# Kernel tuning notes

Hardware: AMD Instinct MI355X
Metric: run time of the kernel (lower is better)

The kernel has to match this reference:

```python
import jax, jax.numpy as jnp
import numpy as np

N_NODES = 100000
N_EDGES = 1600000
D_IN = 128
D_OUT = 5


def setup_inputs() -> dict:
    key = jax.random.key(0)
    k1, k2, k3, k4, k5 = jax.random.split(key, 5)
    x = jax.random.normal(k1, (N_NODES, D_IN), dtype=jnp.float32)
    edge_index = jax.random.randint(k2, (2, N_EDGES), 0, N_NODES, dtype=jnp.int64)
    scale = 1.0 / np.sqrt(D_IN)
    W_l = jax.random.normal(k3, (D_OUT, D_IN), dtype=jnp.float32) * scale
    b_l = jax.random.normal(k4, (D_OUT,), dtype=jnp.float32) * scale
    W_r = jax.random.normal(k5, (D_OUT, D_IN), dtype=jnp.float32) * scale
    return {"x": x, "edge_index": edge_index, "W_l": W_l, "b_l": b_l, "W_r": W_r}


def reference(x, edge_index, W_l, b_l, W_r):
    # PyG SAGEConv with aggr='mean', root_weight=True:
    # out_i = mean_{j: (j->i) in E} x_j @ W_l^T + b_l + x_i @ W_r^T
    n = x.shape[0]
    src = edge_index[0]
    dst = edge_index[1]
    msgs = x[src]  # [E, D_in] gather (irregular access)
    agg_sum = jax.ops.segment_sum(msgs, dst, num_segments=n)  # [N, D_in]
    deg = jax.ops.segment_sum(jnp.ones(src.shape, dtype=x.dtype), dst, num_segments=n)
    agg_mean = agg_sum / jnp.maximum(deg, 1.0)[:, None]  # zero-degree nodes -> 0
    out = agg_mean @ W_l.T + b_l + x @ W_r.T  # [N, D_out]
    return out
```

## Files before the change

### kernel.cpp

```cpp
#include <hip/hip_runtime.h>
#include <hip/hip_bf16.h>


#define N_NODES 100000
#define N_EDGES 1600000
#define D_IN 128
#define D_OUT 5

#define HL_STRIDE 8

#define B_NODES 391
#define N_BUCKETS 256
#define CAP 7168

#define SC_EPT 8
#define SC_EPB (256 * SC_EPT)
#define SC_GRID 782

#define PROJ_NPB 64
#define PROJ_BLOCKS 1564
#define FUSED_GRID 2346

#define FXS 262144.0f
#define FXB 16777216u
#define FXBF 16777216.0f
#define INV_FXS (1.0f / 262144.0f)

typedef unsigned long long u64;
typedef unsigned int u32;

__global__ __launch_bounds__(256) void proj_scatter_kernel(
    const float* __restrict__ x,
    const float* __restrict__ Wl,
    const float* __restrict__ Wr,
    float* __restrict__ hl,
    float* __restrict__ hr,
    const int* __restrict__ ei,
    unsigned int* __restrict__ sorted,
    int* __restrict__ cursor)
{
    __shared__ __align__(16) float smem[1280];
    const int tid = threadIdx.x;
    const int role = blockIdx.x % 3;

    if (role != 2) {
        const int pblk = (blockIdx.x / 3) * 2 + role;

        for (int i = tid; i < 320; i += 256) {
            float4 v = (i < 160) ? ((const float4*)Wl)[i]
                                 : ((const float4*)Wr)[i - 160];
            ((float4*)smem)[i] = v;
        }
        __syncthreads();

        const int g = tid >> 4;
        const int k = tid & 15;
        const float* wk = smem + k * 8;
        const int node0 = pblk * PROJ_NPB + g * 4;

#pragma unroll
        for (int it = 0; it < 4; ++it) {
            const int node = node0 + it;
            if (node < N_NODES) {
                const float4* xr = (const float4*)(x + (size_t)node * D_IN + k * 8);
                float4 x0 = xr[0];
                float4 x1 = xr[1];

                float s[10];
#pragma unroll
                for (int o = 0; o < 10; ++o) {
                    const float4* w4 = (const float4*)(wk + o * 128);
                    float4 w0 = w4[0];
                    float4 w1 = w4[1];
                    s[o] = x0.x * w0.x + x0.y * w0.y + x0.z * w0.z + x0.w * w0.w
                         + x1.x * w1.x + x1.y * w1.y + x1.z * w1.z + x1.w * w1.w;
                }

#pragma unroll
                for (int o = 0; o < 10; ++o) {
                    s[o] += __shfl_xor(s[o], 8, 64);
                    s[o] += __shfl_xor(s[o], 4, 64);
                    s[o] += __shfl_xor(s[o], 2, 64);
                    s[o] += __shfl_xor(s[o], 1, 64);
                }

                if (k == 0) {
                    float* pl = hl + (size_t)node * HL_STRIDE;
                    *(float4*)pl = make_float4(s[0], s[1], s[2], s[3]);
                    pl[4] = s[4];
                    float* pr = hr + (size_t)node * HL_STRIDE;
                    *(float4*)pr = make_float4(s[5], s[6], s[7], s[8]);
                    pr[4] = s[9];
                }
            }
        }
    } else {
        int* hist    = (int*)smem;
        int* basepos = hist + N_BUCKETS;

        if (tid < N_BUCKETS) hist[tid] = 0;
        __syncthreads();

        const int blk = blockIdx.x / 3;
        const int e0  = blk * SC_EPB + tid * SC_EPT;

        int srcv[SC_EPT], dstv[SC_EPT], slot[SC_EPT];
        bool valid[SC_EPT];

        if (e0 + SC_EPT <= N_EDGES) {
            const int4* s4 = (const int4*)(ei + e0);
            const int4* d4 = (const int4*)(ei + N_EDGES + e0);
            int4 sa = s4[0], sb = s4[1], da = d4[0], db = d4[1];
            srcv[0]=sa.x; srcv[1]=sa.y; srcv[2]=sa.z; srcv[3]=sa.w;
            srcv[4]=sb.x; srcv[5]=sb.y; srcv[6]=sb.z; srcv[7]=sb.w;
            dstv[0]=da.x; dstv[1]=da.y; dstv[2]=da.z; dstv[3]=da.w;
            dstv[4]=db.x; dstv[5]=db.y; dstv[6]=db.z; dstv[7]=db.w;
#pragma unroll
            for (int q = 0; q < SC_EPT; ++q) valid[q] = true;
        } else {
#pragma unroll
            for (int q = 0; q < SC_EPT; ++q) {
                int e = e0 + q;
                valid[q] = (e < N_EDGES);
                srcv[q] = valid[q] ? ei[e] : 0;
                dstv[q] = valid[q] ? ei[N_EDGES + e] : 0;
            }
        }

#pragma unroll
        for (int q = 0; q < SC_EPT; ++q) {
            if (valid[q]) {
                unsigned b = (unsigned)dstv[q] / 391u;
                slot[q] = atomicAdd(&hist[b], 1);
            }
        }
        __syncthreads();

        if (tid < N_BUCKETS) {
            int c = hist[tid];
            if (c > 0) basepos[tid] = atomicAdd(&cursor[tid], c);
        }
        __syncthreads();

#pragma unroll
        for (int q = 0; q < SC_EPT; ++q) {
            if (valid[q]) {
                unsigned b = (unsigned)dstv[q] / 391u;
                unsigned r = (unsigned)dstv[q] - b * 391u;
                unsigned rec = (r << 17) | (unsigned)srcv[q];
                sorted[(size_t)b * CAP + basepos[b] + slot[q]] = rec;
            }
        }
    }
}

__global__ __launch_bounds__(1024) void agg_kernel(
    const unsigned int* __restrict__ sorted,
    const int* __restrict__ cursor,
    const float* __restrict__ hl,
    const float* __restrict__ hr,
    const float* __restrict__ bias,
    float* __restrict__ out)
{
    __shared__ u64 acc[B_NODES * 3];

    const int b   = blockIdx.x;
    const int tid = threadIdx.x;

    for (int i = tid; i < B_NODES * 3; i += 1024) acc[i] = 0ull;
    __syncthreads();

    const int cnt = cursor[b];
    const unsigned int* sp = sorted + (size_t)b * CAP;
    const int nvec = cnt >> 2;

    for (int it = tid; it < nvec; it += 1024) {
        uint4 v = ((const uint4*)sp)[it];
        int s0 = (int)(v.x & 0x1FFFFu), r0 = (int)(v.x >> 17);
        int s1 = (int)(v.y & 0x1FFFFu), r1 = (int)(v.y >> 17);
        int s2 = (int)(v.z & 0x1FFFFu), r2 = (int)(v.z >> 17);
        int s3 = (int)(v.w & 0x1FFFFu), r3 = (int)(v.w >> 17);

        const float* p0 = hl + (size_t)s0 * HL_STRIDE;
        const float* p1 = hl + (size_t)s1 * HL_STRIDE;
        const float* p2 = hl + (size_t)s2 * HL_STRIDE;
        const float* p3 = hl + (size_t)s3 * HL_STRIDE;
        float4 h0 = *(const float4*)p0; float e0 = p0[4];
        float4 h1 = *(const float4*)p1; float e1 = p1[4];
        float4 h2 = *(const float4*)p2; float e2 = p2[4];
        float4 h3 = *(const float4*)p3; float e3 = p3[4];

#define EMIT(hh, ee, rr)                                                     \
        {                                                                    \
            u32 f0 = __float2uint_rn(fmaf((hh).x, FXS, FXBF));               \
            u32 f1 = __float2uint_rn(fmaf((hh).y, FXS, FXBF));               \
            u32 f2 = __float2uint_rn(fmaf((hh).z, FXS, FXBF));               \
            u32 f3 = __float2uint_rn(fmaf((hh).w, FXS, FXBF));               \
            u32 f4 = __float2uint_rn(fmaf((ee),   FXS, FXBF));               \
            u64* a = acc + (rr) * 3;                                         \
            atomicAdd(&a[0], ((u64)f1 << 32) | f0);                          \
            atomicAdd(&a[1], ((u64)f3 << 32) | f2);                          \
            atomicAdd(&a[2], ((u64)f4 << 32) | 1u);                          \
        }
        EMIT(h0, e0, r0) EMIT(h1, e1, r1) EMIT(h2, e2, r2) EMIT(h3, e3, r3)
    }
    for (int i = (nvec << 2) + tid; i < cnt; i += 1024) {
        unsigned int v = sp[i];
        int src = (int)(v & 0x1FFFFu);
        int r   = (int)(v >> 17);
        const float* p = hl + (size_t)src * HL_STRIDE;
        float4 h = *(const float4*)p;
        float  e = p[4];
        EMIT(h, e, r)
    }
#undef EMIT
    __syncthreads();

    const int nodebase = b * B_NODES;
    for (int n = tid; n < B_NODES; n += 1024) {
        int node = nodebase + n;
        if (node >= N_NODES) continue;
        u64 w0 = acc[n * 3 + 0];
        u64 w1 = acc[n * 3 + 1];
        u64 w2 = acc[n * 3 + 2];
        u32 deg = (u32)(w2 & 0xFFFFFFFFu);
        u32 db  = deg * FXB;
        int i0 = (int)((u32)(w0 & 0xFFFFFFFFu) - db);
        int i1 = (int)((u32)(w0 >> 32)         - db);
        int i2 = (int)((u32)(w1 & 0xFFFFFFFFu) - db);
        int i3 = (int)((u32)(w1 >> 32)         - db);
        int i4 = (int)((u32)(w2 >> 32)         - db);

        float rec = INV_FXS / fmaxf((float)deg, 1.0f);
        const float* h = hr + (size_t)node * HL_STRIDE;
        float* o = out + (size_t)node * 5;
        o[0] = (float)i0 * rec + bias[0] + h[0];
        o[1] = (float)i1 * rec + bias[1] + h[1];
        o[2] = (float)i2 * rec + bias[2] + h[2];
        o[3] = (float)i3 * rec + bias[3] + h[3];
        o[4] = (float)i4 * rec + bias[4] + h[4];
    }
}

extern "C" void kernel_launch(void* const* d_in, const int* in_sizes, int n_in,
                              void* d_out, int out_size, void* d_ws, size_t ws_size,
                              hipStream_t stream) {
    const float* x    = (const float*)d_in[0];
    const int*   ei   = (const int*)d_in[1];
    const float* Wl   = (const float*)d_in[2];
    const float* bl   = (const float*)d_in[3];
    const float* Wr   = (const float*)d_in[4];
    float*       out  = (float*)d_out;

    float*        hl     = (float*)d_ws;
    float*        hr     = hl + (size_t)N_NODES * HL_STRIDE;
    unsigned int* sorted = (unsigned int*)(hr + (size_t)N_NODES * HL_STRIDE);
    int*          cursor = (int*)(sorted + (size_t)N_BUCKETS * CAP);

    hipMemsetAsync(cursor, 0, N_BUCKETS * sizeof(int), stream);

    proj_scatter_kernel<<<FUSED_GRID, 256, 0, stream>>>(
        x, Wl, Wr, hl, hr, ei, sorted, cursor);

    agg_kernel<<<N_BUCKETS, 1024, 0, stream>>>(sorted, cursor, hl, hr, bl, out);
}
```

Baseline: 145.8 us.

## Fuse projection, bucket scatter and aggregation into one cooperative kernel

Replaces the two-kernel pipeline with a single cooperative launch of 256 blocks of 1024 threads. Each block first projects nodes in a grid-stride loop, then buckets a 6400-edge chunk, then passes a grid-wide sync before aggregating its bucket. This removes the second kernel launch and the gap between kernels. In exchange it runs fewer, larger blocks, reads the weights from global memory instead of shared memory, and adds grid-sync overhead and lower occupancy for the projection phase.

After: 322.9 us. 2.21x slower.

```diff
diff --git a/kernel.cpp b/kernel.cpp
--- a/kernel.cpp
+++ b/kernel.cpp
@@ -1,11 +1,13 @@
 #include <hip/hip_runtime.h>
 #include <hip/hip_bf16.h>
+#include <hip/hip_cooperative_groups.h>
+
+namespace cg = cooperative_groups;
 
 
 #define N_NODES 100000
 #define N_EDGES 1600000
 #define D_IN 128
-#define D_OUT 5
 
 #define HL_STRIDE 8
 
@@ -13,13 +15,10 @@
 #define N_BUCKETS 256
 #define CAP 7168
 
-#define SC_EPT 8
-#define SC_EPB (256 * SC_EPT)
-#define SC_GRID 782
-
-#define PROJ_NPB 64
-#define PROJ_BLOCKS 1564
-#define FUSED_GRID 2346
+#define NBLK 256
+#define NTHR 1024
+#define NGROUPS (NBLK * (NTHR / 16))
+#define EPB 6400
 
 #define FXS 262144.0f
 #define FXB 16777216u
@@ -29,166 +28,137 @@
 typedef unsigned long long u64;
 typedef unsigned int u32;
 
-__global__ __launch_bounds__(256) void proj_scatter_kernel(
+__global__ __launch_bounds__(NTHR, 4) void mega_kernel(
     const float* __restrict__ x,
     const float* __restrict__ Wl,
     const float* __restrict__ Wr,
     float* __restrict__ hl,
     float* __restrict__ hr,
     const int* __restrict__ ei,
-    unsigned int* __restrict__ sorted,
-    int* __restrict__ cursor)
-{
-    __shared__ __align__(16) float smem[1280];
-    const int tid = threadIdx.x;
-    const int role = blockIdx.x % 3;
-
-    if (role != 2) {
-        const int pblk = (blockIdx.x / 3) * 2 + role;
-
-        for (int i = tid; i < 320; i += 256) {
-            float4 v = (i < 160) ? ((const float4*)Wl)[i]
-                                 : ((const float4*)Wr)[i - 160];
-            ((float4*)smem)[i] = v;
-        }
-        __syncthreads();
-
-        const int g = tid >> 4;
-        const int k = tid & 15;
-        const float* wk = smem + k * 8;
-        const int node0 = pblk * PROJ_NPB + g * 4;
-
-#pragma unroll
-        for (int it = 0; it < 4; ++it) {
-            const int node = node0 + it;
-            if (node < N_NODES) {
-                const float4* xr = (const float4*)(x + (size_t)node * D_IN + k * 8);
-                float4 x0 = xr[0];
-                float4 x1 = xr[1];
-
-                float s[10];
-#pragma unroll
-                for (int o = 0; o < 10; ++o) {
-                    const float4* w4 = (const float4*)(wk + o * 128);
-                    float4 w0 = w4[0];
-                    float4 w1 = w4[1];
-                    s[o] = x0.x * w0.x + x0.y * w0.y + x0.z * w0.z + x0.w * w0.w
-                         + x1.x * w1.x + x1.y * w1.y + x1.z * w1.z + x1.w * w1.w;
-                }
-
-#pragma unroll
-                for (int o = 0; o < 10; ++o) {
-                    s[o] += __shfl_xor(s[o], 8, 64);
-                    s[o] += __shfl_xor(s[o], 4, 64);
-                    s[o] += __shfl_xor(s[o], 2, 64);
-                    s[o] += __shfl_xor(s[o], 1, 64);
-                }
-
-                if (k == 0) {
-                    float* pl = hl + (size_t)node * HL_STRIDE;
-                    *(float4*)pl = make_float4(s[0], s[1], s[2], s[3]);
-                    pl[4] = s[4];
-                    float* pr = hr + (size_t)node * HL_STRIDE;
-                    *(float4*)pr = make_float4(s[5], s[6], s[7], s[8]);
-                    pr[4] = s[9];
-                }
-            }
-        }
-    } else {
-        int* hist    = (int*)smem;
-        int* basepos = hist + N_BUCKETS;
-
-        if (tid < N_BUCKETS) hist[tid] = 0;
-        __syncthreads();
-
-        const int blk = blockIdx.x / 3;
-        const int e0  = blk * SC_EPB + tid * SC_EPT;
-
-        int srcv[SC_EPT], dstv[SC_EPT], slot[SC_EPT];
-        bool valid[SC_EPT];
-
-        if (e0 + SC_EPT <= N_EDGES) {
-            const int4* s4 = (const int4*)(ei + e0);
-            const int4* d4 = (const int4*)(ei + N_EDGES + e0);
-            int4 sa = s4[0], sb = s4[1], da = d4[0], db = d4[1];
-            srcv[0]=sa.x; srcv[1]=sa.y; srcv[2]=sa.z; srcv[3]=sa.w;
-            srcv[4]=sb.x; srcv[5]=sb.y; srcv[6]=sb.z; srcv[7]=sb.w;
-            dstv[0]=da.x; dstv[1]=da.y; dstv[2]=da.z; dstv[3]=da.w;
-            dstv[4]=db.x; dstv[5]=db.y; dstv[6]=db.z; dstv[7]=db.w;
-#pragma unroll
-            for (int q = 0; q < SC_EPT; ++q) valid[q] = true;
-        } else {
-#pragma unroll
-            for (int q = 0; q < SC_EPT; ++q) {
-                int e = e0 + q;
-                valid[q] = (e < N_EDGES);
-                srcv[q] = valid[q] ? ei[e] : 0;
-                dstv[q] = valid[q] ? ei[N_EDGES + e] : 0;
-            }
-        }
-
-#pragma unroll
-        for (int q = 0; q < SC_EPT; ++q) {
-            if (valid[q]) {
-                unsigned b = (unsigned)dstv[q] / 391u;
-                slot[q] = atomicAdd(&hist[b], 1);
-            }
-        }
-        __syncthreads();
-
-        if (tid < N_BUCKETS) {
-            int c = hist[tid];
-            if (c > 0) basepos[tid] = atomicAdd(&cursor[tid], c);
-        }
-        __syncthreads();
-
-#pragma unroll
-        for (int q = 0; q < SC_EPT; ++q) {
-            if (valid[q]) {
-                unsigned b = (unsigned)dstv[q] / 391u;
-                unsigned r = (unsigned)dstv[q] - b * 391u;
-                unsigned rec = (r << 17) | (unsigned)srcv[q];
-                sorted[(size_t)b * CAP + basepos[b] + slot[q]] = rec;
-            }
-        }
-    }
-}
-
-__global__ __launch_bounds__(1024) void agg_kernel(
-    const unsigned int* __restrict__ sorted,
-    const int* __restrict__ cursor,
-    const float* __restrict__ hl,
-    const float* __restrict__ hr,
+    u32* __restrict__ sorted,
+    int* __restrict__ cursor,
     const float* __restrict__ bias,
     float* __restrict__ out)
 {
     __shared__ u64 acc[B_NODES * 3];
-
+    int* hist    = (int*)acc;
+    int* basepos = hist + N_BUCKETS;
+
+    const int tid = threadIdx.x;
     const int b   = blockIdx.x;
-    const int tid = threadIdx.x;
-
-    for (int i = tid; i < B_NODES * 3; i += 1024) acc[i] = 0ull;
-    __syncthreads();
-
-    const int cnt = cursor[b];
-    const unsigned int* sp = sorted + (size_t)b * CAP;
-    const int nvec = cnt >> 2;
-
-    for (int it = tid; it < nvec; it += 1024) {
-        uint4 v = ((const uint4*)sp)[it];
-        int s0 = (int)(v.x & 0x1FFFFu), r0 = (int)(v.x >> 17);
-        int s1 = (int)(v.y & 0x1FFFFu), r1 = (int)(v.y >> 17);
-        int s2 = (int)(v.z & 0x1FFFFu), r2 = (int)(v.z >> 17);
-        int s3 = (int)(v.w & 0x1FFFFu), r3 = (int)(v.w >> 17);
-
-        const float* p0 = hl + (size_t)s0 * HL_STRIDE;
-        const float* p1 = hl + (size_t)s1 * HL_STRIDE;
-        const float* p2 = hl + (size_t)s2 * HL_STRIDE;
-        const float* p3 = hl + (size_t)s3 * HL_STRIDE;
-        float4 h0 = *(const float4*)p0; float e0 = p0[4];
-        float4 h1 = *(const float4*)p1; float e1 = p1[4];
-        float4 h2 = *(const float4*)p2; float e2 = p2[4];
-        float4 h3 = *(const float4*)p3; float e3 = p3[4];
+
+    {
+        const int k  = tid & 15;
+        for (int node = b * (NTHR / 16) + (tid >> 4); node < N_NODES;
+             node += NGROUPS) {
+            const float4* xr = (const float4*)(x + (size_t)node * D_IN + k * 8);
+            float4 x0 = xr[0];
+            float4 x1 = xr[1];
+
+            float s[10];
+#pragma unroll
+            for (int o = 0; o < 10; ++o) {
+                const float* w = (o < 5 ? Wl + o * D_IN : Wr + (o - 5) * D_IN) + k * 8;
+                float4 w0 = ((const float4*)w)[0];
+                float4 w1 = ((const float4*)w)[1];
+                s[o] = x0.x * w0.x + x0.y * w0.y + x0.z * w0.z + x0.w * w0.w
+                     + x1.x * w1.x + x1.y * w1.y + x1.z * w1.z + x1.w * w1.w;
+            }
+
+#pragma unroll
+            for (int o = 0; o < 10; ++o) {
+                s[o] += __shfl_xor(s[o], 8, 64);
+                s[o] += __shfl_xor(s[o], 4, 64);
+                s[o] += __shfl_xor(s[o], 2, 64);
+                s[o] += __shfl_xor(s[o], 1, 64);
+            }
+
+            if (k == 0) {
+                float* pl = hl + (size_t)node * HL_STRIDE;
+                *(float4*)pl = make_float4(s[0], s[1], s[2], s[3]);
+                pl[4] = s[4];
+                float* pr = hr + (size_t)node * HL_STRIDE;
+                *(float4*)pr = make_float4(s[5], s[6], s[7], s[8]);
+                pr[4] = s[9];
+            }
+        }
+    }
+
+    {
+        if (tid < N_BUCKETS) hist[tid] = 0;
+        __syncthreads();
+
+        const bool active = (b < N_EDGES / EPB);
+        int sa[8], da[8], slot[8];
+        bool hasB = false;
+
+        if (active) {
+            const int e0 = b * EPB;
+            const int eA = e0 + tid * 4;
+            int4 s4 = *(const int4*)(ei + eA);
+            int4 d4 = *(const int4*)(ei + N_EDGES + eA);
+            sa[0]=s4.x; sa[1]=s4.y; sa[2]=s4.z; sa[3]=s4.w;
+            da[0]=d4.x; da[1]=d4.y; da[2]=d4.z; da[3]=d4.w;
+            hasB = (4096 + tid * 4) < EPB;
+            if (hasB) {
+                const int eB = e0 + 4096 + tid * 4;
+                int4 s5 = *(const int4*)(ei + eB);
+                int4 d5 = *(const int4*)(ei + N_EDGES + eB);
+                sa[4]=s5.x; sa[5]=s5.y; sa[6]=s5.z; sa[7]=s5.w;
+                da[4]=d5.x; da[5]=d5.y; da[6]=d5.z; da[7]=d5.w;
+            }
+
+#pragma unroll
+            for (int q = 0; q < 4; ++q) {
+                unsigned bk = (unsigned)da[q] / 391u;
+                slot[q] = atomicAdd(&hist[bk], 1);
+            }
+            if (hasB) {
+#pragma unroll
+                for (int q = 4; q < 8; ++q) {
+                    unsigned bk = (unsigned)da[q] / 391u;
+                    slot[q] = atomicAdd(&hist[bk], 1);
+                }
+            }
+        }
+        __syncthreads();
+
+        if (tid < N_BUCKETS) {
+            int c = hist[tid];
+            basepos[tid] = (c > 0) ? atomicAdd(&cursor[tid], c) : 0;
+        }
+        __syncthreads();
+
+        if (active) {
+#pragma unroll
+            for (int q = 0; q < 4; ++q) {
+                unsigned bk = (unsigned)da[q] / 391u;
+                unsigned r  = (unsigned)da[q] - bk * 391u;
+                sorted[(size_t)bk * CAP + basepos[bk] + slot[q]] =
+                    (r << 17) | (unsigned)sa[q];
+            }
+            if (hasB) {
+#pragma unroll
+                for (int q = 4; q < 8; ++q) {
+                    unsigned bk = (unsigned)da[q] / 391u;
+                    unsigned r  = (unsigned)da[q] - bk * 391u;
+                    sorted[(size_t)bk * CAP + basepos[bk] + slot[q]] =
+                        (r << 17) | (unsigned)sa[q];
+                }
+            }
+        }
+    }
+
+    __threadfence();
+    cg::this_grid().sync();
+
+    {
+        for (int i = tid; i < B_NODES * 3; i += NTHR) acc[i] = 0ull;
+        __syncthreads();
+
+        const int cnt = cursor[b];
+        const u32* sp = sorted + (size_t)b * CAP;
+        const int nvec = cnt >> 2;
 
 #define EMIT(hh, ee, rr)                                                     \
         {                                                                    \
@@ -202,43 +172,61 @@
             atomicAdd(&a[1], ((u64)f3 << 32) | f2);                          \
             atomicAdd(&a[2], ((u64)f4 << 32) | 1u);                          \
         }
-        EMIT(h0, e0, r0) EMIT(h1, e1, r1) EMIT(h2, e2, r2) EMIT(h3, e3, r3)
-    }
-    for (int i = (nvec << 2) + tid; i < cnt; i += 1024) {
-        unsigned int v = sp[i];
-        int src = (int)(v & 0x1FFFFu);
-        int r   = (int)(v >> 17);
-        const float* p = hl + (size_t)src * HL_STRIDE;
-        float4 h = *(const float4*)p;
-        float  e = p[4];
-        EMIT(h, e, r)
-    }
+
+        for (int it = tid; it < nvec; it += NTHR) {
+            uint4 v = ((const uint4*)sp)[it];
+            int s0 = (int)(v.x & 0x1FFFFu), r0 = (int)(v.x >> 17);
+            int s1 = (int)(v.y & 0x1FFFFu), r1 = (int)(v.y >> 17);
+            int s2 = (int)(v.z & 0x1FFFFu), r2 = (int)(v.z >> 17);
+            int s3 = (int)(v.w & 0x1FFFFu), r3 = (int)(v.w >> 17);
+
+            const float* p0 = hl + (size_t)s0 * HL_STRIDE;
+            const float* p1 = hl + (size_t)s1 * HL_STRIDE;
+            const float* p2 = hl + (size_t)s2 * HL_STRIDE;
+            const float* p3 = hl + (size_t)s3 * HL_STRIDE;
+            float4 h0 = *(const float4*)p0; float e0 = p0[4];
+            float4 h1 = *(const float4*)p1; float e1 = p1[4];
+            float4 h2 = *(const float4*)p2; float e2 = p2[4];
+            float4 h3 = *(const float4*)p3; float e3 = p3[4];
+
+            EMIT(h0, e0, r0) EMIT(h1, e1, r1) EMIT(h2, e2, r2) EMIT(h3, e3, r3)
+        }
+        for (int i = (nvec << 2) + tid; i < cnt; i += NTHR) {
+            u32 v = sp[i];
+            int src = (int)(v & 0x1FFFFu);
+            int r   = (int)(v >> 17);
+            const float* p = hl + (size_t)src * HL_STRIDE;
+            float4 h = *(const float4*)p;
+            float  e = p[4];
+            EMIT(h, e, r)
+        }
 #undef EMIT
-    __syncthreads();
-
-    const int nodebase = b * B_NODES;
-    for (int n = tid; n < B_NODES; n += 1024) {
-        int node = nodebase + n;
-        if (node >= N_NODES) continue;
-        u64 w0 = acc[n * 3 + 0];
-        u64 w1 = acc[n * 3 + 1];
-        u64 w2 = acc[n * 3 + 2];
-        u32 deg = (u32)(w2 & 0xFFFFFFFFu);
-        u32 db  = deg * FXB;
-        int i0 = (int)((u32)(w0 & 0xFFFFFFFFu) - db);
-        int i1 = (int)((u32)(w0 >> 32)         - db);
-        int i2 = (int)((u32)(w1 & 0xFFFFFFFFu) - db);
-        int i3 = (int)((u32)(w1 >> 32)         - db);
-        int i4 = (int)((u32)(w2 >> 32)         - db);
-
-        float rec = INV_FXS / fmaxf((float)deg, 1.0f);
-        const float* h = hr + (size_t)node * HL_STRIDE;
-        float* o = out + (size_t)node * 5;
-        o[0] = (float)i0 * rec + bias[0] + h[0];
-        o[1] = (float)i1 * rec + bias[1] + h[1];
-        o[2] = (float)i2 * rec + bias[2] + h[2];
-        o[3] = (float)i3 * rec + bias[3] + h[3];
-        o[4] = (float)i4 * rec + bias[4] + h[4];
+        __syncthreads();
+
+        const int nodebase = b * B_NODES;
+        for (int n = tid; n < B_NODES; n += NTHR) {
+            int node = nodebase + n;
+            if (node >= N_NODES) continue;
+            u64 w0 = acc[n * 3 + 0];
+            u64 w1 = acc[n * 3 + 1];
+            u64 w2 = acc[n * 3 + 2];
+            u32 deg = (u32)(w2 & 0xFFFFFFFFu);
+            u32 db  = deg * FXB;
+            int i0 = (int)((u32)(w0 & 0xFFFFFFFFu) - db);
+            int i1 = (int)((u32)(w0 >> 32)         - db);
+            int i2 = (int)((u32)(w1 & 0xFFFFFFFFu) - db);
+            int i3 = (int)((u32)(w1 >> 32)         - db);
+            int i4 = (int)((u32)(w2 >> 32)         - db);
+
+            float rec = INV_FXS / fmaxf((float)deg, 1.0f);
+            const float* h = hr + (size_t)node * HL_STRIDE;
+            float* o = out + (size_t)node * 5;
+            o[0] = (float)i0 * rec + bias[0] + h[0];
+            o[1] = (float)i1 * rec + bias[1] + h[1];
+            o[2] = (float)i2 * rec + bias[2] + h[2];
+            o[3] = (float)i3 * rec + bias[3] + h[3];
+            o[4] = (float)i4 * rec + bias[4] + h[4];
+        }
     }
 }
 
@@ -252,15 +240,17 @@
     const float* Wr   = (const float*)d_in[4];
     float*       out  = (float*)d_out;
 
-    float*        hl     = (float*)d_ws;
-    float*        hr     = hl + (size_t)N_NODES * HL_STRIDE;
-    unsigned int* sorted = (unsigned int*)(hr + (size_t)N_NODES * HL_STRIDE);
-    int*          cursor = (int*)(sorted + (size_t)N_BUCKETS * CAP);
+    float* hl   = (float*)d_ws;
+    float* hr   = hl + (size_t)N_NODES * HL_STRIDE;
+    u32*   sorted = (u32*)(hr + (size_t)N_NODES * HL_STRIDE);
+    int*   cursor = (int*)(sorted + (size_t)N_BUCKETS * CAP);
 
     hipMemsetAsync(cursor, 0, N_BUCKETS * sizeof(int), stream);
 
-    proj_scatter_kernel<<<FUSED_GRID, 256, 0, stream>>>(
-        x, Wl, Wr, hl, hr, ei, sorted, cursor);
-
-    agg_kernel<<<N_BUCKETS, 1024, 0, stream>>>(sorted, cursor, hl, hr, bl, out);
+    void* args[] = {
+        (void*)&x, (void*)&Wl, (void*)&Wr, (void*)&hl, (void*)&hr,
+        (void*)&ei, (void*)&sorted, (void*)&cursor, (void*)&bl, (void*)&out
+    };
+    hipLaunchCooperativeKernel((void*)mega_kernel, dim3(NBLK), dim3(NTHR),
+                               args, 0, stream);
 }
```

## Use power-of-two buckets, register-held weights, and split block roles

Applied to the files above, without the earlier changes.

Bucket size changes from 391 to 256 nodes, so bucket and row indices come from a shift and mask instead of integer division. The number of buckets rises to 392 with a smaller capacity each, which gives the aggregation kernel more, smaller blocks. The projection blocks now keep the weights in registers instead of shared memory, and the grid gives projection and scatter blocks contiguous ranges rather than interleaving them. The risks are higher register pressure from 80 weight floats per thread, and bucket overflow if a bucket ever holds more than 5120 edges.

Result: faster. 135.3 us (-7.2%).

```diff
diff --git a/kernel.cpp b/kernel.cpp
--- a/kernel.cpp
+++ b/kernel.cpp
@@ -9,17 +9,18 @@
 
 #define HL_STRIDE 8
 
-#define B_NODES 391
-#define N_BUCKETS 256
-#define CAP 7168
+#define BSHIFT 8
+#define B_NODES 256
+#define N_BUCKETS 392
+#define CAP 5120
 
 #define SC_EPT 8
 #define SC_EPB (256 * SC_EPT)
-#define SC_GRID 782
+#define SC_GRID ((N_EDGES + SC_EPB - 1) / SC_EPB)
 
 #define PROJ_NPB 64
-#define PROJ_BLOCKS 1564
-#define FUSED_GRID 2346
+#define PROJ_BLOCKS ((N_NODES + PROJ_NPB - 1) / PROJ_NPB)
+#define FUSED_GRID (PROJ_BLOCKS + SC_GRID)
 
 #define FXS 262144.0f
 #define FXB 16777216u
@@ -29,7 +30,7 @@
 typedef unsigned long long u64;
 typedef unsigned int u32;
 
-__global__ __launch_bounds__(256) void proj_scatter_kernel(
+__global__ __launch_bounds__(256, 4) void proj_scatter_kernel(
     const float* __restrict__ x,
     const float* __restrict__ Wl,
     const float* __restrict__ Wr,
@@ -39,24 +40,21 @@
     unsigned int* __restrict__ sorted,
     int* __restrict__ cursor)
 {
-    __shared__ __align__(16) float smem[1280];
     const int tid = threadIdx.x;
-    const int role = blockIdx.x % 3;
-
-    if (role != 2) {
-        const int pblk = (blockIdx.x / 3) * 2 + role;
-
-        for (int i = tid; i < 320; i += 256) {
-            float4 v = (i < 160) ? ((const float4*)Wl)[i]
-                                 : ((const float4*)Wr)[i - 160];
-            ((float4*)smem)[i] = v;
-        }
-        __syncthreads();
-
+
+    if (blockIdx.x < PROJ_BLOCKS) {
         const int g = tid >> 4;
         const int k = tid & 15;
-        const float* wk = smem + k * 8;
-        const int node0 = pblk * PROJ_NPB + g * 4;
+
+        float4 wv[10][2];
+#pragma unroll
+        for (int o = 0; o < 10; ++o) {
+            const float* w = (o < 5 ? Wl + o * D_IN : Wr + (o - 5) * D_IN) + k * 8;
+            wv[o][0] = ((const float4*)w)[0];
+            wv[o][1] = ((const float4*)w)[1];
+        }
+
+        const int node0 = blockIdx.x * PROJ_NPB + g * 4;
 
 #pragma unroll
         for (int it = 0; it < 4; ++it) {
@@ -69,11 +67,10 @@
                 float s[10];
 #pragma unroll
                 for (int o = 0; o < 10; ++o) {
-                    const float4* w4 = (const float4*)(wk + o * 128);
-                    float4 w0 = w4[0];
-                    float4 w1 = w4[1];
-                    s[o] = x0.x * w0.x + x0.y * w0.y + x0.z * w0.z + x0.w * w0.w
-                         + x1.x * w1.x + x1.y * w1.y + x1.z * w1.z + x1.w * w1.w;
+                    s[o] = x0.x * wv[o][0].x + x0.y * wv[o][0].y
+                         + x0.z * wv[o][0].z + x0.w * wv[o][0].w
+                         + x1.x * wv[o][1].x + x1.y * wv[o][1].y
+                         + x1.z * wv[o][1].z + x1.w * wv[o][1].w;
                 }
 
 #pragma unroll
@@ -95,13 +92,13 @@
             }
         }
     } else {
-        int* hist    = (int*)smem;
-        int* basepos = hist + N_BUCKETS;
-
-        if (tid < N_BUCKETS) hist[tid] = 0;
+        __shared__ int hist[N_BUCKETS];
+        __shared__ int basepos[N_BUCKETS];
+
+        for (int i = tid; i < N_BUCKETS; i += 256) hist[i] = 0;
         __syncthreads();
 
-        const int blk = blockIdx.x / 3;
+        const int blk = blockIdx.x - PROJ_BLOCKS;
         const int e0  = blk * SC_EPB + tid * SC_EPT;
 
         int srcv[SC_EPT], dstv[SC_EPT], slot[SC_EPT];
@@ -130,24 +127,24 @@
 #pragma unroll
         for (int q = 0; q < SC_EPT; ++q) {
             if (valid[q]) {
-                unsigned b = (unsigned)dstv[q] / 391u;
+                int b = dstv[q] >> BSHIFT;
                 slot[q] = atomicAdd(&hist[b], 1);
             }
         }
         __syncthreads();
 
-        if (tid < N_BUCKETS) {
-            int c = hist[tid];
-            if (c > 0) basepos[tid] = atomicAdd(&cursor[tid], c);
+        for (int b = tid; b < N_BUCKETS; b += 256) {
+            int c = hist[b];
+            if (c > 0) basepos[b] = atomicAdd(&cursor[b], c);
         }
         __syncthreads();
 
 #pragma unroll
         for (int q = 0; q < SC_EPT; ++q) {
             if (valid[q]) {
-                unsigned b = (unsigned)dstv[q] / 391u;
-                unsigned r = (unsigned)dstv[q] - b * 391u;
-                unsigned rec = (r << 17) | (unsigned)srcv[q];
+                int b = dstv[q] >> BSHIFT;
+                int r = dstv[q] & (B_NODES - 1);
+                unsigned int rec = ((unsigned int)r << 17) | (unsigned int)srcv[q];
                 sorted[(size_t)b * CAP + basepos[b] + slot[q]] = rec;
             }
         }
@@ -174,6 +171,19 @@
     const unsigned int* sp = sorted + (size_t)b * CAP;
     const int nvec = cnt >> 2;
 
+#define EMIT(hh, ee, rr)                                                     \
+    {                                                                        \
+        u32 f0 = __float2uint_rn(fmaf((hh).x, FXS, FXBF));                   \
+        u32 f1 = __float2uint_rn(fmaf((hh).y, FXS, FXBF));                   \
+        u32 f2 = __float2uint_rn(fmaf((hh).z, FXS, FXBF));                   \
+        u32 f3 = __float2uint_rn(fmaf((hh).w, FXS, FXBF));                   \
+        u32 f4 = __float2uint_rn(fmaf((ee),   FXS, FXBF));                   \
+        u64* a = acc + (rr) * 3;                                             \
+        atomicAdd(&a[0], ((u64)f1 << 32) | f0);                              \
+        atomicAdd(&a[1], ((u64)f3 << 32) | f2);                              \
+        atomicAdd(&a[2], ((u64)f4 << 32) | 1u);                              \
+    }
+
     for (int it = tid; it < nvec; it += 1024) {
         uint4 v = ((const uint4*)sp)[it];
         int s0 = (int)(v.x & 0x1FFFFu), r0 = (int)(v.x >> 17);
@@ -190,18 +200,6 @@
         float4 h2 = *(const float4*)p2; float e2 = p2[4];
         float4 h3 = *(const float4*)p3; float e3 = p3[4];
 
-#define EMIT(hh, ee, rr)                                                     \
-        {                                                                    \
-            u32 f0 = __float2uint_rn(fmaf((hh).x, FXS, FXBF));               \
-            u32 f1 = __float2uint_rn(fmaf((hh).y, FXS, FXBF));               \
-            u32 f2 = __float2uint_rn(fmaf((hh).z, FXS, FXBF));               \
-            u32 f3 = __float2uint_rn(fmaf((hh).w, FXS, FXBF));               \
-            u32 f4 = __float2uint_rn(fmaf((ee),   FXS, FXBF));               \
-            u64* a = acc + (rr) * 3;                                         \
-            atomicAdd(&a[0], ((u64)f1 << 32) | f0);                          \
-            atomicAdd(&a[1], ((u64)f3 << 32) | f2);                          \
-            atomicAdd(&a[2], ((u64)f4 << 32) | 1u);                          \
-        }
         EMIT(h0, e0, r0) EMIT(h1, e1, r1) EMIT(h2, e2, r2) EMIT(h3, e3, r3)
     }
     for (int i = (nvec << 2) + tid; i < cnt; i += 1024) {
@@ -216,7 +214,7 @@
 #undef EMIT
     __syncthreads();
 
-    const int nodebase = b * B_NODES;
+    const int nodebase = b << BSHIFT;
     for (int n = tid; n < B_NODES; n += 1024) {
         int node = nodebase + n;
         if (node >= N_NODES) continue;
```
